# Kernel tuning notes

Measured on AMD Instinct MI355X. Metric: run time of the kernel, lower is better.

The kernel has to match this reference:

```python
import jax, jax.numpy as jnp
import numpy as np

B, T, C, H, L, V = 2, 1024, 768, 12, 12, 50257
D = C // H  # head size = 64
EPS = 1e-5


def _layer_norm(x, w, b):
    m = x.mean(-1, keepdims=True)
    v = x.var(-1, keepdims=True)
    return (x - m) * jax.lax.rsqrt(v + EPS) * w + b


def setup_inputs() -> dict:
    key = jax.random.key(0)
    ks = jax.random.split(key, 8)
    std = 0.02
    res_std = 0.02 * (2 * L) ** -0.5  # NANOGPT_SCALE_INIT
    rn = lambda k, shape, s: jax.random.normal(k, shape, jnp.float32) * s
    return dict(
        idx=jax.random.randint(ks[0], (B, T), 0, V),
        wte=rn(ks[1], (V, C), std),
        wpe=rn(ks[2], (T, C), std),
        ln1_w=jnp.ones((L, C), jnp.float32), ln1_b=jnp.zeros((L, C), jnp.float32),
        qkv_w=rn(ks[3], (L, C, 3 * C), std), qkv_b=jnp.zeros((L, 3 * C), jnp.float32),
        proj_w=rn(ks[4], (L, C, C), res_std), proj_b=jnp.zeros((L, C), jnp.float32),
        ln2_w=jnp.ones((L, C), jnp.float32), ln2_b=jnp.zeros((L, C), jnp.float32),
        fc_w=rn(ks[5], (L, C, 4 * C), std), fc_b=jnp.zeros((L, 4 * C), jnp.float32),
        fco_w=rn(ks[6], (L, 4 * C, C), res_std), fco_b=jnp.zeros((L, C), jnp.float32),
        lnf_w=jnp.ones((C,), jnp.float32), lnf_b=jnp.zeros((C,), jnp.float32),
    )


def reference(idx, wte, wpe, ln1_w, ln1_b, qkv_w, qkv_b, proj_w, proj_b,
              ln2_w, ln2_b, fc_w, fc_b, fco_w, fco_b, lnf_w, lnf_b):
    x = wte[idx] + wpe[:T]  # [B, T, C] tok + pos emb
    mask = jnp.tril(jnp.ones((T, T), bool))  # causal
    scale = 1.0 / np.sqrt(D).astype(np.float32)

    def block(x, p):
        l1w, l1b, qw, qb, pw, pb, l2w, l2b, fw, fb, fow, fob = p
        h = _layer_norm(x, l1w, l1b)
        qkv = h @ qw + qb  # [B, T, 3C]
        q, k, v = jnp.split(qkv, 3, axis=-1)
        q = q.reshape(B, T, H, D)
        k = k.reshape(B, T, H, D)
        v = v.reshape(B, T, H, D)
        att = jnp.einsum('bqhd,bkhd->bhqk', q, k) * scale
        att = jnp.where(mask, att, -jnp.inf)
        att = jax.nn.softmax(att, axis=-1)
        y = jnp.einsum('bhqk,bkhd->bqhd', att, v).reshape(B, T, C)
        x = x + y @ pw + pb
        h2 = _layer_norm(x, l2w, l2b)
        x = x + jax.nn.gelu(h2 @ fw + fb, approximate=True) @ fow + fob
        return x, None

    x, _ = jax.lax.scan(block, x, (ln1_w, ln1_b, qkv_w, qkv_b, proj_w, proj_b,
                                   ln2_w, ln2_b, fc_w, fc_b, fco_w, fco_b))
    x = _layer_norm(x, lnf_w, lnf_b)
    logits = x @ wte.T  # tied lm_head
    return logits
```

## Files before the change

### kernel.cpp

```cpp
#include <hip/hip_runtime.h>
#include <cmath>
#include <cstdint>

#define T_SEQ 1024
#define NH 12
#define NL 12
#define NV 50257
#define CD 768
#define M_ROWS 2048

typedef __bf16 bf16_t;
typedef __bf16 bf16x8 __attribute__((ext_vector_type(8)));
typedef float f32x4 __attribute__((ext_vector_type(4)));

__device__ __forceinline__ void gload16(const bf16_t* g, bf16_t* l) {
  __builtin_amdgcn_global_load_lds(
      (const __attribute__((address_space(1))) void*)g,
      (__attribute__((address_space(3))) void*)l, 16, 0, 0);
}

__global__ __launch_bounds__(256) void embed_k(const int* __restrict__ idx,
    const float* __restrict__ wte, const float* __restrict__ wpe,
    float* __restrict__ x) {
  int m = blockIdx.x;
  int t = m & (T_SEQ - 1);
  int tok = idx[m];
  const float* a = wte + (size_t)tok * CD;
  const float* p = wpe + (size_t)t * CD;
  float* xr = x + (size_t)m * CD;
  int c = threadIdx.x;
  xr[c]       = a[c]       + p[c];
  xr[c + 256] = a[c + 256] + p[c + 256];
  xr[c + 512] = a[c + 512] + p[c + 512];
}

__global__ __launch_bounds__(256) void cvt_k(const float* __restrict__ in,
    bf16_t* __restrict__ out, int n4) {
  int i = blockIdx.x * 256 + threadIdx.x;
  if (i < n4) {
    float4 v = ((const float4*)in)[i];
    bf16_t* o = out + (size_t)i * 4;
    o[0] = (bf16_t)v.x; o[1] = (bf16_t)v.y;
    o[2] = (bf16_t)v.z; o[3] = (bf16_t)v.w;
  }
}

__global__ __launch_bounds__(256) void transcvt_k(const float* __restrict__ W0,
    bf16_t* __restrict__ WT0, int K, int N) {
  const float* W = W0 + (size_t)blockIdx.z * K * N;
  bf16_t* WT = WT0 + (size_t)blockIdx.z * N * K;
  __shared__ float tl[32][33];
  int k0 = blockIdx.y * 32, n0 = blockIdx.x * 32;
  int j = threadIdx.x & 31, i0 = threadIdx.x >> 5;
  #pragma unroll
  for (int i = i0; i < 32; i += 8) tl[i][j] = W[(size_t)(k0 + i) * N + n0 + j];
  __syncthreads();
  #pragma unroll
  for (int i = i0; i < 32; i += 8)
    WT[(size_t)(n0 + i) * K + k0 + j] = (bf16_t)tl[j][i];
}

__global__ __launch_bounds__(256) void ln_k(const float* __restrict__ x,
    const float* __restrict__ w, const float* __restrict__ bi,
    bf16_t* __restrict__ out) {
  int row = blockIdx.x;
  const float* xr = x + (size_t)row * CD;
  int t = threadIdx.x;
  float v0 = xr[t], v1 = xr[t + 256], v2 = xr[t + 512];
  float s = v0 + v1 + v2;
  float ss = v0 * v0 + v1 * v1 + v2 * v2;
  #pragma unroll
  for (int o = 1; o < 64; o <<= 1) { s += __shfl_xor(s, o); ss += __shfl_xor(ss, o); }
  __shared__ float sh[8];
  int wid = t >> 6, lane = t & 63;
  if (lane == 0) { sh[wid] = s; sh[4 + wid] = ss; }
  __syncthreads();
  s  = sh[0] + sh[1] + sh[2] + sh[3];
  ss = sh[4] + sh[5] + sh[6] + sh[7];
  float mean = s * (1.f / CD);
  float var  = ss * (1.f / CD) - mean * mean;
  float rs = rsqrtf(var + 1e-5f);
  bf16_t* orow = out + (size_t)row * CD;
  orow[t]       = (bf16_t)((v0 - mean) * rs * w[t]       + bi[t]);
  orow[t + 256] = (bf16_t)((v1 - mean) * rs * w[t + 256] + bi[t + 256]);
  orow[t + 512] = (bf16_t)((v2 - mean) * rs * w[t + 512] + bi[t + 512]);
}

template <int BM, int BN, int EPI, bool SWAP, bool XSWZ>
__global__ __launch_bounds__(256) void gemm_bt(
    const bf16_t* __restrict__ A,
    const bf16_t* __restrict__ BT,
    const float* __restrict__ bias,
    const float* __restrict__ resid,
    void* __restrict__ out_p,
    int Mdim, int Ndim, int Kdim) {
  constexpr int MR = BM / 32, NR = BN / 32;
  constexpr int LPW = (BM + BN) / 64;
  __shared__ __align__(1024) bf16_t As[3][BM * 32];
  __shared__ __align__(1024) bf16_t Bs[3][BN * 32];
  const int t = threadIdx.x;
  const int wid = t >> 6, lane = t & 63;
  const int wm = wid >> 1, wn = wid & 1;
  int bx = blockIdx.x, by = blockIdx.y;
  if (XSWZ) {
    int gx = gridDim.x;
    int lin = by * gx + bx;
    int cpx = (gx * gridDim.y) >> 3;
    int swz = (lin & 7) * cpx + (lin >> 3);
    bx = swz % gx; by = swz / gx;
  }
  const int m0 = (SWAP ? bx : by) * BM;
  const int n0 = (SWAP ? by : bx) * BN;
  const int l15 = lane & 15, lhi = lane >> 4;

  const int srow = lane >> 2;
  const int schk = lane & 3;

  auto stage = [&](int bi, int kt) {
    #pragma unroll
    for (int i = 0; i < BM / 64; ++i) {
      int rbase = wid * (BM / 4) + i * 16;
      int r = rbase + srow;
      int c = schk ^ ((r >> 1) & 3);
      gload16(A + (size_t)(m0 + r) * Kdim + kt + c * 8, &As[bi][rbase * 32]);
    }
    #pragma unroll
    for (int i = 0; i < BN / 64; ++i) {
      int rbase = wid * (BN / 4) + i * 16;
      int r = rbase + srow;
      int nr = n0 + r; if (nr >= Ndim) nr = Ndim - 1;
      int c = schk ^ ((r >> 1) & 3);
      gload16(BT + (size_t)nr * Kdim + kt + c * 8, &Bs[bi][rbase * 32]);
    }
  };

  f32x4 acc[MR][NR] = {};
  const int NT = Kdim >> 5;

  stage(0, 0);
  if (NT > 1) stage(1, 32);
  for (int tt = 0; tt < NT; ++tt) {
    if (tt < NT - 1) asm volatile("s_waitcnt vmcnt(%0)" :: "i"(LPW) : "memory");
    else             asm volatile("s_waitcnt vmcnt(0)" ::: "memory");
    __builtin_amdgcn_sched_barrier(0);
    __builtin_amdgcn_s_barrier();
    __builtin_amdgcn_sched_barrier(0);

    const bf16_t* Ab = As[tt % 3];
    const bf16_t* Bb = Bs[tt % 3];
    bf16x8 af[MR], bfr[NR];
    #pragma unroll
    for (int mm = 0; mm < MR; ++mm) {
      int ra = wm * (BM / 2) + mm * 16 + l15;
      af[mm] = *(const bf16x8*)&Ab[ra * 32 + ((lhi ^ (ra >> 1)) & 3) * 8];
    }
    #pragma unroll
    for (int nn = 0; nn < NR; ++nn) {
      int rb = wn * (BN / 2) + nn * 16 + l15;
      bfr[nn] = *(const bf16x8*)&Bb[rb * 32 + ((lhi ^ (rb >> 1)) & 3) * 8];
    }
    if (tt + 2 < NT) stage((tt + 2) % 3, (tt + 2) * 32);

    __builtin_amdgcn_s_setprio(1);
    #pragma unroll
    for (int mm = 0; mm < MR; ++mm)
      #pragma unroll
      for (int nn = 0; nn < NR; ++nn)
        acc[mm][nn] = __builtin_amdgcn_mfma_f32_16x16x32_bf16(af[mm], bfr[nn], acc[mm][nn], 0, 0, 0);
    __builtin_amdgcn_s_setprio(0);

    __builtin_amdgcn_sched_barrier(0);
    __builtin_amdgcn_s_barrier();
    __builtin_amdgcn_sched_barrier(0);
  }

  bf16_t* ob = (bf16_t*)out_p;
  float*  of = (float*)out_p;
  const int row0 = m0 + wm * (BM / 2);
  const int col0 = n0 + wn * (BN / 2);
  #pragma unroll
  for (int mm = 0; mm < MR; ++mm) {
    #pragma unroll
    for (int nn = 0; nn < NR; ++nn) {
      int col = col0 + nn * 16 + l15;
      if (col >= Ndim) continue;
      float bv = (EPI != 3) ? bias[col] : 0.f;
      #pragma unroll
      for (int r = 0; r < 4; ++r) {
        int row = row0 + mm * 16 + lhi * 4 + r;
        float v = acc[mm][nn][r] + bv;
        size_t o = (size_t)row * Ndim + col;
        if (EPI == 0) {
          ob[o] = (bf16_t)v;
        } else if (EPI == 1) {
          float u = v + 0.044715f * v * v * v;
          v = 0.5f * v * (1.f + tanhf(0.79788456080286536f * u));
          ob[o] = (bf16_t)v;
        } else if (EPI == 2) {
          of[o] = resid[o] + v;
        } else {
          of[o] = v;
        }
      }
    }
  }
}

__global__ __launch_bounds__(256) void vtrans_k(const bf16_t* __restrict__ qkv,
                                                bf16_t* __restrict__ VT) {
  __shared__ __align__(16) bf16_t tl[64 * 72];
  const int bh = blockIdx.y;
  const int t0 = blockIdx.x * 64;
  const int b = bh / NH, h = bh % NH;
  const int tid = threadIdx.x;
  const int row = tid >> 2;
  const int seg = (tid & 3) * 16;

  const bf16_t* src = qkv + (size_t)(b * T_SEQ + t0 + row) * (3 * CD) + 2 * CD + h * 64 + seg;
  bf16x8 v0 = *(const bf16x8*)src;
  bf16x8 v1 = *(const bf16x8*)(src + 8);
  #pragma unroll
  for (int j = 0; j < 8; ++j) tl[(seg + j) * 72 + row] = v0[j];
  #pragma unroll
  for (int j = 0; j < 8; ++j) tl[(seg + 8 + j) * 72 + row] = v1[j];
  __syncthreads();

  bf16_t* dst = VT + ((size_t)bh * 64 + row) * T_SEQ + t0 + seg;
  *(bf16x8*)dst       = *(const bf16x8*)&tl[row * 72 + seg];
  *(bf16x8*)(dst + 8) = *(const bf16x8*)&tl[row * 72 + seg + 8];
}

__global__ __launch_bounds__(64) void attn_k(const bf16_t* __restrict__ qkv,
                                             const bf16_t* __restrict__ VT,
                                             bf16_t* __restrict__ y) {
  __shared__ __align__(16) bf16_t Ps[16 * 40];
  const int lane = threadIdx.x;
  const int gw = blockIdx.x;
  const int qi = gw & 63;
  const int bh = gw >> 6;
  const int h = bh % NH, b = bh / NH;
  const bf16_t* Qbase = qkv + (size_t)b * T_SEQ * (3 * CD) + h * 64;
  const bf16_t* Kbase = Qbase + CD;
  const bf16_t* Vt = VT + (size_t)bh * 64 * T_SEQ;

  const int l15 = lane & 15, lhi = lane >> 4;
  const int q0 = qi * 16;

  bf16x8 aq[2];
  #pragma unroll
  for (int c = 0; c < 2; ++c)
    aq[c] = *(const bf16x8*)(Qbase + (size_t)(q0 + l15) * (3 * CD) + c * 32 + lhi * 8);

  f32x4 acc[4] = {};
  float m_[4], l_[4];
  #pragma unroll
  for (int r = 0; r < 4; ++r) { m_[r] = -INFINITY; l_[r] = 0.f; }

  const int qrow = q0 + lhi * 4;
  const int nt = (q0 + 47) / 32;
  for (int kt = 0; kt < nt; ++kt) {
    const int k0 = kt * 32;
    f32x4 s[2] = {};
    #pragma unroll
    for (int c = 0; c < 2; ++c) {
      #pragma unroll
      for (int kc = 0; kc < 2; ++kc) {
        bf16x8 bk = *(const bf16x8*)(Kbase + (size_t)(k0 + kc * 16 + l15) * (3 * CD) + c * 32 + lhi * 8);
        s[kc] = __builtin_amdgcn_mfma_f32_16x16x32_bf16(aq[c], bk, s[kc], 0, 0, 0);
      }
    }
    float mx[4];
    #pragma unroll
    for (int r = 0; r < 4; ++r) mx[r] = -INFINITY;
    #pragma unroll
    for (int kc = 0; kc < 2; ++kc) {
      const int kcol = k0 + kc * 16 + l15;
      #pragma unroll
      for (int r = 0; r < 4; ++r) {
        float sv = (kcol <= qrow + r) ? s[kc][r] * 0.125f : -INFINITY;
        s[kc][r] = sv;
        mx[r] = fmaxf(mx[r], sv);
      }
    }
    #pragma unroll
    for (int r = 0; r < 4; ++r) {
      mx[r] = fmaxf(mx[r], __shfl_xor(mx[r], 1));
      mx[r] = fmaxf(mx[r], __shfl_xor(mx[r], 2));
      mx[r] = fmaxf(mx[r], __shfl_xor(mx[r], 4));
      mx[r] = fmaxf(mx[r], __shfl_xor(mx[r], 8));
    }
    float al[4], rs[4];
    #pragma unroll
    for (int r = 0; r < 4; ++r) {
      float mn = fmaxf(m_[r], mx[r]);
      al[r] = __expf(m_[r] - mn);
      m_[r] = mn;
      float p0 = __expf(s[0][r] - mn);
      float p1 = __expf(s[1][r] - mn);
      s[0][r] = p0; s[1][r] = p1;
      rs[r] = p0 + p1;
    }
    #pragma unroll
    for (int r = 0; r < 4; ++r) {
      rs[r] += __shfl_xor(rs[r], 1);
      rs[r] += __shfl_xor(rs[r], 2);
      rs[r] += __shfl_xor(rs[r], 4);
      rs[r] += __shfl_xor(rs[r], 8);
      l_[r] = l_[r] * al[r] + rs[r];
    }
    #pragma unroll
    for (int dt = 0; dt < 4; ++dt)
      #pragma unroll
      for (int r = 0; r < 4; ++r) acc[dt][r] *= al[r];
    #pragma unroll
    for (int kc = 0; kc < 2; ++kc)
      #pragma unroll
      for (int r = 0; r < 4; ++r)
        Ps[(lhi * 4 + r) * 40 + kc * 16 + l15] = (bf16_t)s[kc][r];
    bf16x8 pa = *(const bf16x8*)&Ps[l15 * 40 + lhi * 8];
    #pragma unroll
    for (int dt = 0; dt < 4; ++dt) {
      bf16x8 bv = *(const bf16x8*)(Vt + (size_t)(dt * 16 + l15) * T_SEQ + k0 + lhi * 8);
      acc[dt] = __builtin_amdgcn_mfma_f32_16x16x32_bf16(pa, bv, acc[dt], 0, 0, 0);
    }
  }
  #pragma unroll
  for (int dt = 0; dt < 4; ++dt)
    #pragma unroll
    for (int r = 0; r < 4; ++r)
      y[(size_t)(b * T_SEQ + q0 + lhi * 4 + r) * CD + h * 64 + dt * 16 + l15] =
          (bf16_t)(acc[dt][r] / l_[r]);
}

extern "C" void kernel_launch(void* const* d_in, const int* in_sizes, int n_in,
                              void* d_out, int out_size, void* d_ws, size_t ws_size,
                              hipStream_t stream) {
  const int*   idx   = (const int*)d_in[0];
  const float* wte   = (const float*)d_in[1];
  const float* wpe   = (const float*)d_in[2];
  const float* ln1w  = (const float*)d_in[3];
  const float* ln1b  = (const float*)d_in[4];
  const float* qkvw  = (const float*)d_in[5];
  const float* qkvb  = (const float*)d_in[6];
  const float* projw = (const float*)d_in[7];
  const float* projb = (const float*)d_in[8];
  const float* ln2w  = (const float*)d_in[9];
  const float* ln2b  = (const float*)d_in[10];
  const float* fcw   = (const float*)d_in[11];
  const float* fcb   = (const float*)d_in[12];
  const float* fcow  = (const float*)d_in[13];
  const float* fcob  = (const float*)d_in[14];
  const float* lnfw  = (const float*)d_in[15];
  const float* lnfb  = (const float*)d_in[16];
  float* out = (float*)d_out;

  char* w = (char*)d_ws;
  auto alloc = [&](size_t bytes) {
    char* p = w; w += (bytes + 255) & ~(size_t)255; return p;
  };
  float*  x    = (float*)alloc((size_t)M_ROWS * CD * 4);
  float*  x2   = (float*)alloc((size_t)M_ROWS * CD * 4);
  bf16_t* hb   = (bf16_t*)alloc((size_t)M_ROWS * CD * 2);
  bf16_t* qkvB = (bf16_t*)alloc((size_t)M_ROWS * 3 * CD * 2);
  bf16_t* yb   = (bf16_t*)alloc((size_t)M_ROWS * CD * 2);
  bf16_t* fca  = (bf16_t*)alloc((size_t)M_ROWS * 4 * CD * 2);
  bf16_t* VT   = (bf16_t*)alloc((size_t)2 * NH * 64 * T_SEQ * 2);
  bf16_t* wteB = (bf16_t*)alloc((size_t)NV * CD * 2);
  bf16_t* wqT_s = (bf16_t*)alloc((size_t)3 * CD * CD * 2);
  bf16_t* wpT_s = (bf16_t*)alloc((size_t)CD * CD * 2);
  bf16_t* wfT_s = (bf16_t*)alloc((size_t)4 * CD * CD * 2);
  bf16_t* woT_s = (bf16_t*)alloc((size_t)CD * 4 * CD * 2);
  const size_t qkvSz = (size_t)3 * CD * CD, prSz = (size_t)CD * CD;
  const size_t fcSz  = (size_t)4 * CD * CD, foSz = (size_t)CD * 4 * CD;
  bf16_t* wqT_b = (bf16_t*)alloc(NL * qkvSz * 2);
  bf16_t* wpT_b = (bf16_t*)alloc(NL * prSz * 2);
  bf16_t* wfT_b = (bf16_t*)alloc(NL * fcSz * 2);
  bf16_t* woT_b = (bf16_t*)alloc(NL * foSz * 2);
  const bool big = (size_t)(w - (char*)d_ws) <= ws_size;

  embed_k<<<M_ROWS, 256, 0, stream>>>(idx, wte, wpe, x);
  {
    int n4 = NV * CD / 4;
    cvt_k<<<(n4 + 255) / 256, 256, 0, stream>>>(wte, wteB, n4);
  }
  if (big) {
    transcvt_k<<<dim3(3 * CD / 32, CD / 32, NL), 256, 0, stream>>>(qkvw,  wqT_b, CD, 3 * CD);
    transcvt_k<<<dim3(CD / 32, CD / 32, NL),     256, 0, stream>>>(projw, wpT_b, CD, CD);
    transcvt_k<<<dim3(4 * CD / 32, CD / 32, NL), 256, 0, stream>>>(fcw,   wfT_b, CD, 4 * CD);
    transcvt_k<<<dim3(CD / 32, 4 * CD / 32, NL), 256, 0, stream>>>(fcow,  woT_b, 4 * CD, CD);
  }

  for (int l = 0; l < NL; ++l) {
    bf16_t *wqT, *wpT, *wfT, *woT;
    if (big) {
      wqT = wqT_b + (size_t)l * qkvSz; wpT = wpT_b + (size_t)l * prSz;
      wfT = wfT_b + (size_t)l * fcSz;  woT = woT_b + (size_t)l * foSz;
    } else {
      wqT = wqT_s; wpT = wpT_s; wfT = wfT_s; woT = woT_s;
      transcvt_k<<<dim3(3 * CD / 32, CD / 32, 1), 256, 0, stream>>>(qkvw  + (size_t)l * CD * 3 * CD, wqT, CD, 3 * CD);
      transcvt_k<<<dim3(CD / 32, CD / 32, 1),     256, 0, stream>>>(projw + (size_t)l * CD * CD,     wpT, CD, CD);
      transcvt_k<<<dim3(4 * CD / 32, CD / 32, 1), 256, 0, stream>>>(fcw   + (size_t)l * CD * 4 * CD, wfT, CD, 4 * CD);
      transcvt_k<<<dim3(CD / 32, 4 * CD / 32, 1), 256, 0, stream>>>(fcow  + (size_t)l * 4 * CD * CD, woT, 4 * CD, CD);
    }

    ln_k<<<M_ROWS, 256, 0, stream>>>(x, ln1w + l * CD, ln1b + l * CD, hb);
    gemm_bt<128, 128, 0, false, false><<<dim3(3 * CD / 128, M_ROWS / 128), 256, 0, stream>>>(
        hb, wqT, qkvb + l * 3 * CD, nullptr, qkvB, M_ROWS, 3 * CD, CD);
    vtrans_k<<<dim3(T_SEQ / 64, 2 * NH), 256, 0, stream>>>(qkvB, VT);
    attn_k<<<2 * NH * 64, 64, 0, stream>>>(qkvB, VT, yb);
    gemm_bt<64, 64, 2, false, false><<<dim3(CD / 64, M_ROWS / 64), 256, 0, stream>>>(
        yb, wpT, projb + l * CD, x, x2, M_ROWS, CD, CD);
    ln_k<<<M_ROWS, 256, 0, stream>>>(x2, ln2w + l * CD, ln2b + l * CD, hb);
    gemm_bt<128, 128, 1, false, false><<<dim3(4 * CD / 128, M_ROWS / 128), 256, 0, stream>>>(
        hb, wfT, fcb + l * 4 * CD, nullptr, fca, M_ROWS, 4 * CD, CD);
    gemm_bt<64, 64, 2, false, false><<<dim3(CD / 64, M_ROWS / 64), 256, 0, stream>>>(
        fca, woT, fcob + l * CD, x2, x, M_ROWS, CD, 4 * CD);
  }

  ln_k<<<M_ROWS, 256, 0, stream>>>(x, lnfw, lnfb, hb);
  gemm_bt<128, 128, 3, true, true><<<dim3(16, (NV + 127) / 128), 256, 0, stream>>>(
      hb, wteB, nullptr, nullptr, out, M_ROWS, NV, CD);
}
```

Measured before the change: 2.322 ms.

## Add dedicated 256x256 LM-head GEMM kernel and widen attention key tiles to 64

```diff
diff --git a/kernel.cpp b/kernel.cpp
--- a/kernel.cpp
+++ b/kernel.cpp
@@ -86,7 +86,7 @@
   orow[t + 512] = (bf16_t)((v2 - mean) * rs * w[t + 512] + bi[t + 512]);
 }
 
-template <int BM, int BN, int EPI, bool SWAP, bool XSWZ>
+template <int BM, int BN, int EPI>
 __global__ __launch_bounds__(256) void gemm_bt(
     const bf16_t* __restrict__ A,
     const bf16_t* __restrict__ BT,
@@ -101,16 +101,7 @@
   const int t = threadIdx.x;
   const int wid = t >> 6, lane = t & 63;
   const int wm = wid >> 1, wn = wid & 1;
-  int bx = blockIdx.x, by = blockIdx.y;
-  if (XSWZ) {
-    int gx = gridDim.x;
-    int lin = by * gx + bx;
-    int cpx = (gx * gridDim.y) >> 3;
-    int swz = (lin & 7) * cpx + (lin >> 3);
-    bx = swz % gx; by = swz / gx;
-  }
-  const int m0 = (SWAP ? bx : by) * BM;
-  const int n0 = (SWAP ? by : bx) * BN;
+  const int m0 = blockIdx.y * BM, n0 = blockIdx.x * BN;
   const int l15 = lane & 15, lhi = lane >> 4;
 
   const int srow = lane >> 2;
@@ -206,6 +197,98 @@
   }
 }
 
+#define LMH_GY 197
+__global__ __launch_bounds__(512, 2) void gemm_lm(
+    const bf16_t* __restrict__ A,
+    const bf16_t* __restrict__ BT,
+    float* __restrict__ out) {
+  __shared__ __align__(1024) bf16_t As[4][256 * 32];
+  __shared__ __align__(1024) bf16_t Bs[4][256 * 32];
+  const int t = threadIdx.x;
+  const int wid = t >> 6, lane = t & 63;
+  const int wr = wid >> 2, wc = wid & 3;
+  const int l15 = lane & 15, lhi = lane >> 4;
+  const int srow = lane >> 2;
+  const int schk = lane & 3;
+
+  int lin = blockIdx.x;
+  int swz = (lin & 7) * LMH_GY + (lin >> 3);
+  const int m0 = (swz & 7) * 256;
+  const int n0 = (swz >> 3) * 256;
+
+  auto stage = [&](int bi, int kt) {
+    #pragma unroll
+    for (int hf = 0; hf < 2; ++hf) {
+      int rb = hf * 128 + wid * 16;
+      int r = rb + srow;
+      int c = schk ^ ((r >> 1) & 3);
+      gload16(A + (size_t)(m0 + r) * CD + kt * 32 + c * 8, &As[bi][rb * 32]);
+    }
+    #pragma unroll
+    for (int hf = 0; hf < 2; ++hf) {
+      int rb = hf * 128 + wid * 16;
+      int r = rb + srow;
+      int nr = n0 + r; if (nr >= NV) nr = NV - 1;
+      int c = schk ^ ((r >> 1) & 3);
+      gload16(BT + (size_t)nr * CD + kt * 32 + c * 8, &Bs[bi][rb * 32]);
+    }
+  };
+
+  f32x4 acc[8][4] = {};
+  const int NT = CD / 32;
+
+  stage(0, 0); stage(1, 1); stage(2, 2);
+  for (int tt = 0; tt < NT; ++tt) {
+    if (tt < NT - 2)       asm volatile("s_waitcnt vmcnt(8)" ::: "memory");
+    else if (tt == NT - 2) asm volatile("s_waitcnt vmcnt(4)" ::: "memory");
+    else                   asm volatile("s_waitcnt vmcnt(0)" ::: "memory");
+    __builtin_amdgcn_sched_barrier(0);
+    __builtin_amdgcn_s_barrier();
+    __builtin_amdgcn_sched_barrier(0);
+
+    const bf16_t* Ab = As[tt & 3];
+    const bf16_t* Bb = Bs[tt & 3];
+    bf16x8 af[8], bfr[4];
+    #pragma unroll
+    for (int mm = 0; mm < 8; ++mm) {
+      int ra = wr * 128 + mm * 16 + l15;
+      af[mm] = *(const bf16x8*)&Ab[ra * 32 + ((lhi ^ (ra >> 1)) & 3) * 8];
+    }
+    #pragma unroll
+    for (int nn = 0; nn < 4; ++nn) {
+      int rb = wc * 64 + nn * 16 + l15;
+      bfr[nn] = *(const bf16x8*)&Bb[rb * 32 + ((lhi ^ (rb >> 1)) & 3) * 8];
+    }
+    if (tt + 3 < NT) stage((tt + 3) & 3, tt + 3);
+
+    __builtin_amdgcn_s_setprio(1);
+    #pragma unroll
+    for (int mm = 0; mm < 8; ++mm)
+      #pragma unroll
+      for (int nn = 0; nn < 4; ++nn)
+        acc[mm][nn] = __builtin_amdgcn_mfma_f32_16x16x32_bf16(af[mm], bfr[nn], acc[mm][nn], 0, 0, 0);
+    __builtin_amdgcn_s_setprio(0);
+
+    __builtin_amdgcn_sched_barrier(0);
+    __builtin_amdgcn_s_barrier();
+    __builtin_amdgcn_sched_barrier(0);
+  }
+
+  const int row0 = m0 + wr * 128;
+  const int col0 = n0 + wc * 64;
+  #pragma unroll
+  for (int mm = 0; mm < 8; ++mm) {
+    #pragma unroll
+    for (int nn = 0; nn < 4; ++nn) {
+      int col = col0 + nn * 16 + l15;
+      if (col >= NV) continue;
+      #pragma unroll
+      for (int r = 0; r < 4; ++r)
+        out[(size_t)(row0 + mm * 16 + lhi * 4 + r) * NV + col] = acc[mm][nn][r];
+    }
+  }
+}
+
 __global__ __launch_bounds__(256) void vtrans_k(const bf16_t* __restrict__ qkv,
                                                 bf16_t* __restrict__ VT) {
   __shared__ __align__(16) bf16_t tl[64 * 72];
@@ -233,7 +316,7 @@
 __global__ __launch_bounds__(64) void attn_k(const bf16_t* __restrict__ qkv,
                                              const bf16_t* __restrict__ VT,
                                              bf16_t* __restrict__ y) {
-  __shared__ __align__(16) bf16_t Ps[16 * 40];
+  __shared__ __align__(16) bf16_t Ps[16 * 72];
   const int lane = threadIdx.x;
   const int gw = blockIdx.x;
   const int qi = gw & 63;
@@ -257,14 +340,14 @@
   for (int r = 0; r < 4; ++r) { m_[r] = -INFINITY; l_[r] = 0.f; }
 
   const int qrow = q0 + lhi * 4;
-  const int nt = (q0 + 47) / 32;
+  const int nt = (q0 + 79) / 64;
   for (int kt = 0; kt < nt; ++kt) {
-    const int k0 = kt * 32;
-    f32x4 s[2] = {};
+    const int k0 = kt * 64;
+    f32x4 s[4] = {};
     #pragma unroll
     for (int c = 0; c < 2; ++c) {
       #pragma unroll
-      for (int kc = 0; kc < 2; ++kc) {
+      for (int kc = 0; kc < 4; ++kc) {
         bf16x8 bk = *(const bf16x8*)(Kbase + (size_t)(k0 + kc * 16 + l15) * (3 * CD) + c * 32 + lhi * 8);
         s[kc] = __builtin_amdgcn_mfma_f32_16x16x32_bf16(aq[c], bk, s[kc], 0, 0, 0);
       }
@@ -273,7 +356,7 @@
     #pragma unroll
     for (int r = 0; r < 4; ++r) mx[r] = -INFINITY;
     #pragma unroll
-    for (int kc = 0; kc < 2; ++kc) {
+    for (int kc = 0; kc < 4; ++kc) {
       const int kcol = k0 + kc * 16 + l15;
       #pragma unroll
       for (int r = 0; r < 4; ++r) {
@@ -297,8 +380,10 @@
       m_[r] = mn;
       float p0 = __expf(s[0][r] - mn);
       float p1 = __expf(s[1][r] - mn);
-      s[0][r] = p0; s[1][r] = p1;
-      rs[r] = p0 + p1;
+      float p2 = __expf(s[2][r] - mn);
+      float p3 = __expf(s[3][r] - mn);
+      s[0][r] = p0; s[1][r] = p1; s[2][r] = p2; s[3][r] = p3;
+      rs[r] = (p0 + p1) + (p2 + p3);
     }
     #pragma unroll
     for (int r = 0; r < 4; ++r) {
@@ -313,15 +398,18 @@
       #pragma unroll
       for (int r = 0; r < 4; ++r) acc[dt][r] *= al[r];
     #pragma unroll
-    for (int kc = 0; kc < 2; ++kc)
+    for (int kc = 0; kc < 4; ++kc)
       #pragma unroll
       for (int r = 0; r < 4; ++r)
-        Ps[(lhi * 4 + r) * 40 + kc * 16 + l15] = (bf16_t)s[kc][r];
-    bf16x8 pa = *(const bf16x8*)&Ps[l15 * 40 + lhi * 8];
-    #pragma unroll
-    for (int dt = 0; dt < 4; ++dt) {
-      bf16x8 bv = *(const bf16x8*)(Vt + (size_t)(dt * 16 + l15) * T_SEQ + k0 + lhi * 8);
-      acc[dt] = __builtin_amdgcn_mfma_f32_16x16x32_bf16(pa, bv, acc[dt], 0, 0, 0);
+        Ps[(lhi * 4 + r) * 72 + kc * 16 + l15] = (bf16_t)s[kc][r];
+    #pragma unroll
+    for (int ks = 0; ks < 2; ++ks) {
+      bf16x8 pa = *(const bf16x8*)&Ps[l15 * 72 + ks * 32 + lhi * 8];
+      #pragma unroll
+      for (int dt = 0; dt < 4; ++dt) {
+        bf16x8 bv = *(const bf16x8*)(Vt + (size_t)(dt * 16 + l15) * T_SEQ + k0 + ks * 32 + lhi * 8);
+        acc[dt] = __builtin_amdgcn_mfma_f32_16x16x32_bf16(pa, bv, acc[dt], 0, 0, 0);
+      }
     }
   }
   #pragma unroll
@@ -358,14 +446,14 @@
   auto alloc = [&](size_t bytes) {
     char* p = w; w += (bytes + 255) & ~(size_t)255; return p;
   };
-  float*  x    = (float*)alloc((size_t)M_ROWS * CD * 4);
-  float*  x2   = (float*)alloc((size_t)M_ROWS * CD * 4);
-  bf16_t* hb   = (bf16_t*)alloc((size_t)M_ROWS * CD * 2);
-  bf16_t* qkvB = (bf16_t*)alloc((size_t)M_ROWS * 3 * CD * 2);
-  bf16_t* yb   = (bf16_t*)alloc((size_t)M_ROWS * CD * 2);
-  bf16_t* fca  = (bf16_t*)alloc((size_t)M_ROWS * 4 * CD * 2);
-  bf16_t* VT   = (bf16_t*)alloc((size_t)2 * NH * 64 * T_SEQ * 2);
-  bf16_t* wteB = (bf16_t*)alloc((size_t)NV * CD * 2);
+  float*  x     = (float*)alloc((size_t)M_ROWS * CD * 4);
+  float*  x2    = (float*)alloc((size_t)M_ROWS * CD * 4);
+  bf16_t* hb    = (bf16_t*)alloc((size_t)M_ROWS * CD * 2);
+  bf16_t* qkvB  = (bf16_t*)alloc((size_t)M_ROWS * 3 * CD * 2);
+  bf16_t* yb    = (bf16_t*)alloc((size_t)M_ROWS * CD * 2);
+  bf16_t* fca   = (bf16_t*)alloc((size_t)M_ROWS * 4 * CD * 2);
+  bf16_t* VT    = (bf16_t*)alloc((size_t)2 * NH * 64 * T_SEQ * 2);
+  bf16_t* wteB  = (bf16_t*)alloc((size_t)NV * CD * 2);
   bf16_t* wqT_s = (bf16_t*)alloc((size_t)3 * CD * CD * 2);
   bf16_t* wpT_s = (bf16_t*)alloc((size_t)CD * CD * 2);
   bf16_t* wfT_s = (bf16_t*)alloc((size_t)4 * CD * CD * 2);
@@ -404,20 +492,19 @@
     }
 
     ln_k<<<M_ROWS, 256, 0, stream>>>(x, ln1w + l * CD, ln1b + l * CD, hb);
-    gemm_bt<128, 128, 0, false, false><<<dim3(3 * CD / 128, M_ROWS / 128), 256, 0, stream>>>(
+    gemm_bt<128, 128, 0><<<dim3(3 * CD / 128, M_ROWS / 128), 256, 0, stream>>>(
         hb, wqT, qkvb + l * 3 * CD, nullptr, qkvB, M_ROWS, 3 * CD, CD);
     vtrans_k<<<dim3(T_SEQ / 64, 2 * NH), 256, 0, stream>>>(qkvB, VT);
     attn_k<<<2 * NH * 64, 64, 0, stream>>>(qkvB, VT, yb);
-    gemm_bt<64, 64, 2, false, false><<<dim3(CD / 64, M_ROWS / 64), 256, 0, stream>>>(
+    gemm_bt<64, 64, 2><<<dim3(CD / 64, M_ROWS / 64), 256, 0, stream>>>(
         yb, wpT, projb + l * CD, x, x2, M_ROWS, CD, CD);
     ln_k<<<M_ROWS, 256, 0, stream>>>(x2, ln2w + l * CD, ln2b + l * CD, hb);
-    gemm_bt<128, 128, 1, false, false><<<dim3(4 * CD / 128, M_ROWS / 128), 256, 0, stream>>>(
+    gemm_bt<128, 128, 1><<<dim3(4 * CD / 128, M_ROWS / 128), 256, 0, stream>>>(
         hb, wfT, fcb + l * 4 * CD, nullptr, fca, M_ROWS, 4 * CD, CD);
-    gemm_bt<64, 64, 2, false, false><<<dim3(CD / 64, M_ROWS / 64), 256, 0, stream>>>(
+    gemm_bt<64, 64, 2><<<dim3(CD / 64, M_ROWS / 64), 256, 0, stream>>>(
         fca, woT, fcob + l * CD, x2, x, M_ROWS, CD, 4 * CD);
   }
 
   ln_k<<<M_ROWS, 256, 0, stream>>>(x, lnfw, lnfb, hb);
-  gemm_bt<128, 128, 3, true, true><<<dim3(16, (NV + 127) / 128), 256, 0, stream>>>(
-      hb, wteB, nullptr, nullptr, out, M_ROWS, NV, CD);
-}
+  gemm_lm<<<8 * LMH_GY, 512, 0, stream>>>(hb, wteB, out);
+}
```

After: 2.458 ms. 5.8% more time.
